# Kernel optimization log

Hardware: AMD Instinct MI355X
Metric: run time of the kernel (lower is better)

The kernel has to match this reference:

```python
import jax, jax.numpy as jnp
import numpy as np

B, L, H, E = 16, 4096, 8, 64
K = 64  # topk modes
SCALE = 1.0 / (512 * 512)  # 1/(in_channels*out_channels)


def setup_inputs() -> dict:
    key = jax.random.key(0)
    k1, k2, k3 = jax.random.split(key, 3)
    q = jax.random.normal(k1, (B, L, H, E), dtype=jnp.float32)
    k = jnp.zeros((B, L, H, E), jnp.float32)  # unused by module
    v = jnp.zeros((B, L, H, E), jnp.float32)  # unused by module
    mask = jnp.zeros((1,), jnp.int32)         # unused by module
    w_real = jax.random.uniform(k2, (K, H, E, E), dtype=jnp.float32) * SCALE
    w_imag = jax.random.uniform(k3, (K, H, E, E), dtype=jnp.float32) * SCALE
    return {"q": q, "k": k, "v": v, "w_real": w_real, "w_imag": w_imag, "mask": mask}


def reference(q, k, v, w_real, w_imag, mask):
    # x_ft: (B, F, H, Ein) complex64, F = L//2 + 1
    x_ft = jnp.fft.rfft(q.astype(jnp.float32), axis=1)
    F = x_ft.shape[1]
    kk = w_real.shape[0]
    # energy score per bin: sum |.|^2 over Ein, mean over batch, mean over heads
    e = (x_ft.real ** 2 + x_ft.imag ** 2).sum(-1)      # (B, F, H)
    score = e.mean(0).mean(-1)                          # (F,)
    score = score.at[0].set(-jnp.inf)                   # topk_exclude_dc=True
    _, idx = jax.lax.top_k(score, kk)                   # sorted desc by energy
    # gather selected modes: (B, K, H, Ein)
    x_sel = x_ft[:, idx]
    w = jax.lax.complex(w_real, w_imag)                 # (K, H, Ein, Eout)
    out_sel = jnp.einsum('bkhe,khef->bkhf', x_sel, w)   # per-head complex matmul
    # packed scatter: selected modes written into the first K bins of zero spectrum
    out_ft = jnp.zeros((x_ft.shape[0], F, x_ft.shape[2], w.shape[-1]), jnp.complex64)
    out_ft = out_ft.at[:, :kk].set(out_sel)
    # inverse FFT back to time domain, norm='backward' (default)
    return jnp.fft.irfft(out_ft, n=q.shape[1], axis=1)
```

## Files before the change

### kernel.cpp

```cpp
#include <hip/hip_runtime.h>


#define NTHREADS 256

__device__ inline void lds_barrier() {
    asm volatile("s_waitcnt lgkmcnt(0)" ::: "memory");
    __builtin_amdgcn_s_barrier();
}

#define ZI(i) ((i) ^ ((((i) >> 4) & 7) << 1))

__device__ inline float2 f2add(float2 a, float2 b) { return make_float2(a.x + b.x, a.y + b.y); }
__device__ inline float2 f2sub(float2 a, float2 b) { return make_float2(a.x - b.x, a.y - b.y); }
__device__ inline float2 cmulf(float2 a, float2 b) {
    return make_float2(__builtin_fmaf(a.x, b.x, -(a.y * b.y)),
                       __builtin_fmaf(a.x, b.y,  a.y * b.x));
}

__device__ inline void radix8(float2& u0, float2& u1, float2& u2, float2& u3,
                              float2& u4, float2& u5, float2& u6, float2& u7,
                              float2 wA, float2 wB, float2 wC) {
    float2 t1 = cmulf(wA, u1), t3 = cmulf(wA, u3), t5 = cmulf(wA, u5), t7 = cmulf(wA, u7);
    float2 a0 = f2add(u0, t1), a1 = f2sub(u0, t1);
    float2 a2 = f2add(u2, t3), a3 = f2sub(u2, t3);
    float2 a4 = f2add(u4, t5), a5 = f2sub(u4, t5);
    float2 a6 = f2add(u6, t7), a7 = f2sub(u6, t7);
    float2 s2 = cmulf(wB, a2), s3 = cmulf(wB, a3);
    float2 s6 = cmulf(wB, a6), s7 = cmulf(wB, a7);
    float2 b0 = f2add(a0, s2), b2 = f2sub(a0, s2);
    float2 b1 = make_float2(a1.x + s3.y, a1.y - s3.x);
    float2 b3 = make_float2(a1.x - s3.y, a1.y + s3.x);
    float2 b4 = f2add(a4, s6), b6 = f2sub(a4, s6);
    float2 b5 = make_float2(a5.x + s7.y, a5.y - s7.x);
    float2 b7 = make_float2(a5.x - s7.y, a5.y + s7.x);
    const float2 C8 = make_float2(0.70710678118654752f, -0.70710678118654752f);
    float2 wC1 = cmulf(wC, C8);
    float2 r4 = cmulf(wC, b4);
    float2 r5 = cmulf(wC1, b5);
    float2 r6t = cmulf(wC, b6);  float2 r6 = make_float2(r6t.y, -r6t.x);
    float2 r7t = cmulf(wC1, b7); float2 r7 = make_float2(r7t.y, -r7t.x);
    u0 = f2add(b0, r4); u4 = f2sub(b0, r4);
    u1 = f2add(b1, r5); u5 = f2sub(b1, r5);
    u2 = f2add(b2, r6); u6 = f2sub(b2, r6);
    u3 = f2add(b3, r7); u7 = f2sub(b3, r7);
}

__global__ void k_tables(float2* __restrict__ trig) {
    int k = blockIdx.x * blockDim.x + threadIdx.x;
    if (k < 4096) {
        double th = (6.283185307179586476925286766559 * (double)k) / 4096.0;
        trig[k] = make_float2((float)cos(th), (float)sin(th));
    }
}

__global__ __launch_bounds__(256) void k_xpose(const float* __restrict__ q,
                                               float2* __restrict__ T) {
    __shared__ float tile[128][65];

    const int tid = threadIdx.x;
    const int bi  = blockIdx.x;
    const int b   = bi >> 8;
    const int h   = (bi >> 5) & 7;
    const int c5  = bi & 31;

    const float* qb = q + ((size_t)b * 4096 * 512) + (size_t)h * 64;
#pragma unroll
    for (int i = 0; i < 8; ++i) {
        const int f = tid + 256 * i;
        const int t = f >> 4, e4 = f & 15;
        const float4 v = *(const float4*)(qb + (size_t)(c5 + 32 * t) * 512 + e4 * 4);
        tile[t][e4 * 4 + 0] = v.x;
        tile[t][e4 * 4 + 1] = v.y;
        tile[t][e4 * 4 + 2] = v.z;
        tile[t][e4 * 4 + 3] = v.w;
    }
    lds_barrier();

    const int wave = tid >> 6, lane = tid & 63;
    const int rl  = __brev(lane) >> 26;
    const int r5c = __brev(c5) >> 27;
    for (int cc = wave; cc < 32; cc += 4) {
        const int eo = cc >> 2, p = cc & 3;
        const int col0 = eo * 8 + 2 * p;
        float2* dst = T + ((size_t)((b * 8 + h) * 8 + eo)) * 16384 + (size_t)p * 4096
                        + (size_t)r5c * 128;
        float4 o;
        o.x = tile[rl][col0];      o.y = tile[rl][col0 + 1];
        o.z = tile[rl + 64][col0]; o.w = tile[rl + 64][col0 + 1];
        *(float4*)(dst + 2 * lane) = o;
    }
}

__global__ __launch_bounds__(256) void k_fft(const float2* __restrict__ trig,
                                             float2* __restrict__ Xout,
                                             unsigned long long* __restrict__ score) {
    __shared__ float2 z[4096];
    __shared__ float2 ctw[216];

    const int tid = threadIdx.x;
    const int bi  = blockIdx.x;

    if (tid < 72) {
        int off, j, sA;
        if (tid < 8) { off = 0;  j = tid;     sA = 8; }
        else         { off = 24; j = tid - 8; sA = 5; }
        float2 a = trig[j << sA], b = trig[j << (sA - 1)], c = trig[j << (sA - 2)];
        ctw[off + 3 * j + 0] = make_float2(a.x, -a.y);
        ctw[off + 3 * j + 1] = make_float2(b.x, -b.y);
        ctw[off + 3 * j + 2] = make_float2(c.x, -c.y);
    }

    float eaccr[8];
#pragma unroll
    for (int k = 0; k < 8; ++k) eaccr[k] = 0.f;

    const float2 ONE = make_float2(1.0f, 0.0f);
    const float2* base = Xout + (size_t)bi * 16384;

    float4 pre[2][4];
#pragma unroll
    for (int it = 0; it < 2; ++it) {
        const int t = tid + 256 * it;
#pragma unroll
        for (int g = 0; g < 4; ++g) pre[it][g] = *(const float4*)(base + 8 * t + 2 * g);
    }
    lds_barrier();

    for (int p = 0; p < 4; ++p) {
        float4 cur[2][4];
#pragma unroll
        for (int it = 0; it < 2; ++it)
#pragma unroll
            for (int g = 0; g < 4; ++g) cur[it][g] = pre[it][g];

        if (p < 3) {
            const float2* pn = base + (size_t)(p + 1) * 4096;
#pragma unroll
            for (int it = 0; it < 2; ++it) {
                const int t = tid + 256 * it;
#pragma unroll
                for (int g = 0; g < 4; ++g) pre[it][g] = *(const float4*)(pn + 8 * t + 2 * g);
            }
        }

#pragma unroll
        for (int it = 0; it < 2; ++it) {
            const int t = tid + 256 * it;
            float2 u0 = make_float2(cur[it][0].x, cur[it][0].y);
            float2 u1 = make_float2(cur[it][0].z, cur[it][0].w);
            float2 u2 = make_float2(cur[it][1].x, cur[it][1].y);
            float2 u3 = make_float2(cur[it][1].z, cur[it][1].w);
            float2 u4 = make_float2(cur[it][2].x, cur[it][2].y);
            float2 u5 = make_float2(cur[it][2].z, cur[it][2].w);
            float2 u6 = make_float2(cur[it][3].x, cur[it][3].y);
            float2 u7 = make_float2(cur[it][3].z, cur[it][3].w);
            radix8(u0, u1, u2, u3, u4, u5, u6, u7, ONE, ONE, ONE);
            const int i0 = 8 * t;
            z[ZI(i0 + 0)] = u0; z[ZI(i0 + 1)] = u1; z[ZI(i0 + 2)] = u2; z[ZI(i0 + 3)] = u3;
            z[ZI(i0 + 4)] = u4; z[ZI(i0 + 5)] = u5; z[ZI(i0 + 6)] = u6; z[ZI(i0 + 7)] = u7;
        }
        lds_barrier();

#pragma unroll
        for (int p8 = 1; p8 <= 3; ++p8) {
            const int st  = 1 + 3 * p8;
            const int h   = 1 << (st - 1);
            for (int t = tid; t < 512; t += NTHREADS) {
                const int j = t & (h - 1);
                const int g = t >> (st - 1);
                const int i0 = (g << (st + 2)) + j;
                int a0 = ZI(i0),         a1 = ZI(i0 + h),     a2 = ZI(i0 + 2 * h), a3 = ZI(i0 + 3 * h);
                int a4 = ZI(i0 + 4 * h), a5 = ZI(i0 + 5 * h), a6 = ZI(i0 + 6 * h), a7 = ZI(i0 + 7 * h);
                float2 u0 = z[a0], u1 = z[a1], u2 = z[a2], u3 = z[a3];
                float2 u4 = z[a4], u5 = z[a5], u6 = z[a6], u7 = z[a7];
                float2 wA, wB, wC;
                if (p8 < 3) {
                    const int off = (p8 == 1) ? 0 : 24;
                    wA = ctw[off + 3 * j + 0];
                    wB = ctw[off + 3 * j + 1];
                    wC = ctw[off + 3 * j + 2];
                } else {
                    float2 a = trig[j << 2], b = trig[j << 1], c = trig[j];
                    wA = make_float2(a.x, -a.y);
                    wB = make_float2(b.x, -b.y);
                    wC = make_float2(c.x, -c.y);
                }
                radix8(u0, u1, u2, u3, u4, u5, u6, u7, wA, wB, wC);
                z[a0] = u0; z[a1] = u1; z[a2] = u2; z[a3] = u3;
                z[a4] = u4; z[a5] = u5; z[a6] = u6; z[a7] = u7;
            }
            lds_barrier();
        }

        {
            const size_t s0 = (size_t)bi * 16384 + (size_t)p * 4096;
#pragma unroll
            for (int k = 0; k < 8; ++k) {
                const int t = tid + 256 * k;
                const int m = t + 1;
                float2 Za = z[ZI(m)];
                float2 Zb = z[ZI(4096 - m)];
                float Xr0 = 0.5f * (Za.x + Zb.x);
                float Xi0 = 0.5f * (Za.y - Zb.y);
                float Xr1 = 0.5f * (Za.y + Zb.y);
                float Xi1 = 0.5f * (Zb.x - Za.x);
                Xout[s0 + t]        = make_float2(Xr0, Xi0);
                Xout[s0 + 2048 + t] = make_float2(Xr1, Xi1);
                eaccr[k] += Xr0 * Xr0 + Xi0 * Xi0 + Xr1 * Xr1 + Xi1 * Xi1;
            }
        }
        lds_barrier();
    }

#pragma unroll
    for (int k = 0; k < 8; ++k) {
        unsigned long long v = (unsigned long long)llrintf(eaccr[k] * 1048576.0f);
        atomicAdd(&score[tid + 256 * k], v);
    }
}

__global__ __launch_bounds__(256) void k_topk(const unsigned long long* __restrict__ score,
                                              int* __restrict__ idx) {
    __shared__ unsigned long long s[2048];
    const int tid = threadIdx.x;
    for (int t = tid; t < 2048; t += 256) s[t] = score[t];
    __syncthreads();

    const int t = blockIdx.x * 256 + tid;
    const unsigned long long my = s[t];
    int rank = 0;
#pragma unroll 8
    for (int u = 0; u < 2048; ++u) {
        unsigned long long o = s[u];
        rank += (int)((o > my) || (o == my && u < t));
    }
    if (rank < 64) idx[rank] = t + 1;
}

__global__ __launch_bounds__(256) void k_proj(const float2* __restrict__ X,
                                              const float* __restrict__ wr,
                                              const float* __restrict__ wi,
                                              const int* __restrict__ idx,
                                              float2* __restrict__ Y) {
    __shared__ float2 xs[16 * 64];
    __shared__ float  wrs[64 * 64];
    __shared__ float  wis[64 * 64];

    const int tid = threadIdx.x;
    const int j = blockIdx.x >> 3;
    const int h = blockIdx.x & 7;
    const int m = idx[j];

    for (int t = tid; t < 1024; t += NTHREADS) {
        int b = t >> 6, e = t & 63;
        xs[t] = X[((size_t)((b * 8 + h) * 64 + e)) * 2048 + (size_t)(m - 1)];
    }
    const float* wrb = wr + ((size_t)(j * 8 + h)) * 4096;
    const float* wib = wi + ((size_t)(j * 8 + h)) * 4096;
    for (int t = tid; t < 4096; t += NTHREADS) { wrs[t] = wrb[t]; wis[t] = wib[t]; }
    lds_barrier();

    const int b  = tid >> 4;
    const int fg = tid & 15;
    for (int fo = 0; fo < 4; ++fo) {
        int f = fg * 4 + fo;
        float yr = 0.f, yi = 0.f;
        for (int e = 0; e < 64; ++e) {
            float2 x = xs[b * 64 + e];
            float a = wrs[e * 64 + f], c = wis[e * 64 + f];
            yr = __builtin_fmaf(x.x, a, yr); yr = __builtin_fmaf(-x.y, c, yr);
            yi = __builtin_fmaf(x.x, c, yi); yi = __builtin_fmaf( x.y, a, yi);
        }
        Y[((size_t)b * 64 + j) * 512 + (size_t)(h * 64 + f)] = make_float2(yr, yi);
    }
}

__global__ __launch_bounds__(256, 4) void k_synth(const float2* __restrict__ Y,
                                                  const float2* __restrict__ trig,
                                                  float* __restrict__ out) {
    __shared__ __align__(16) float2 ys[64][32];

    const int tid = threadIdx.x;
    const int bi  = blockIdx.x;
    const int b   = bi >> 8;
    const int hft = (bi >> 4) & 15;
    const int lt  = bi & 15;

    const float invN = 1.0f / 4096.0f;
    const float2* yb = Y + (size_t)b * 64 * 512 + (size_t)hft * 32;
    for (int t = tid; t < 64 * 32; t += NTHREADS) {
        int j = t >> 5, cc = t & 31;
        float2 y = yb[(size_t)j * 512 + cc];
        if (j == 0) ys[0][cc] = make_float2(y.x * invN, 0.0f);
        else        ys[j][cc] = make_float2(y.x * (2.0f * invN), y.y * (2.0f * invN));
    }
    lds_barrier();

    const int r = tid >> 3;
    const int c = tid & 7;
    const int l0 = lt * 64 + r * 2;

    float2 rot[2], w[2];
#pragma unroll
    for (int v = 0; v < 2; ++v) {
        w[v] = trig[(l0 + v) & 4095];
        rot[v] = make_float2(1.0f, 0.0f);
    }

    float F0[2][4], F1[2][4], F2[2][4], F3[2][4], H1[2][4], H3[2][4];
#pragma unroll
    for (int v = 0; v < 2; ++v)
#pragma unroll
        for (int u = 0; u < 4; ++u) {
            F0[v][u] = F1[v][u] = F2[v][u] = F3[v][u] = 0.0f;
            H1[v][u] = H3[v][u] = 0.0f;
        }

#define LOAD_YV(JROW)                                                        \
    float2 yv[4];                                                            \
    {                                                                        \
        const float4 ta = *(const float4*)&ys[(JROW)][c * 2];                \
        const float4 tb = *(const float4*)&ys[(JROW)][c * 2 + 16];           \
        yv[0] = make_float2(ta.x, ta.y); yv[1] = make_float2(ta.z, ta.w);    \
        yv[2] = make_float2(tb.x, tb.y); yv[3] = make_float2(tb.z, tb.w);    \
    }

    for (int j = 0; j < 64; j += 4) {
        {
            LOAD_YV(j)
#pragma unroll
            for (int v = 0; v < 2; ++v) {
                const float cx = rot[v].x, sx = rot[v].y;
#pragma unroll
                for (int u = 0; u < 4; ++u) {
                    float a = F0[v][u];
                    a = __builtin_fmaf(cx, yv[u].x, a);
                    a = __builtin_fmaf(-sx, yv[u].y, a);
                    F0[v][u] = a;
                }
                float nx = __builtin_fmaf(rot[v].x, w[v].x, -(rot[v].y * w[v].y));
                float ny = __builtin_fmaf(rot[v].x, w[v].y,  (rot[v].y * w[v].x));
                rot[v] = make_float2(nx, ny);
            }
        }
        {
            LOAD_YV(j + 1)
#pragma unroll
            for (int v = 0; v < 2; ++v) {
                const float cx = rot[v].x, sx = rot[v].y;
#pragma unroll
                for (int u = 0; u < 4; ++u) {
                    float a = F1[v][u], g = H1[v][u];
                    a = __builtin_fmaf(cx, yv[u].x, a);
                    a = __builtin_fmaf(-sx, yv[u].y, a);
                    g = __builtin_fmaf(sx, yv[u].x, g);
                    g = __builtin_fmaf(cx, yv[u].y, g);
                    F1[v][u] = a; H1[v][u] = g;
                }
                float nx = __builtin_fmaf(rot[v].x, w[v].x, -(rot[v].y * w[v].y));
                float ny = __builtin_fmaf(rot[v].x, w[v].y,  (rot[v].y * w[v].x));
                rot[v] = make_float2(nx, ny);
            }
        }
        {
            LOAD_YV(j + 2)
#pragma unroll
            for (int v = 0; v < 2; ++v) {
                const float cx = rot[v].x, sx = rot[v].y;
#pragma unroll
                for (int u = 0; u < 4; ++u) {
                    float a = F2[v][u];
                    a = __builtin_fmaf(cx, yv[u].x, a);
                    a = __builtin_fmaf(-sx, yv[u].y, a);
                    F2[v][u] = a;
                }
                float nx = __builtin_fmaf(rot[v].x, w[v].x, -(rot[v].y * w[v].y));
                float ny = __builtin_fmaf(rot[v].x, w[v].y,  (rot[v].y * w[v].x));
                rot[v] = make_float2(nx, ny);
            }
        }
        {
            LOAD_YV(j + 3)
#pragma unroll
            for (int v = 0; v < 2; ++v) {
                const float cx = rot[v].x, sx = rot[v].y;
#pragma unroll
                for (int u = 0; u < 4; ++u) {
                    float a = F3[v][u], g = H3[v][u];
                    a = __builtin_fmaf(cx, yv[u].x, a);
                    a = __builtin_fmaf(-sx, yv[u].y, a);
                    g = __builtin_fmaf(sx, yv[u].x, g);
                    g = __builtin_fmaf(cx, yv[u].y, g);
                    F3[v][u] = a; H3[v][u] = g;
                }
                float nx = __builtin_fmaf(rot[v].x, w[v].x, -(rot[v].y * w[v].y));
                float ny = __builtin_fmaf(rot[v].x, w[v].y,  (rot[v].y * w[v].x));
                rot[v] = make_float2(nx, ny);
            }
        }
    }
#undef LOAD_YV

#pragma unroll
    for (int v = 0; v < 2; ++v) {
        float* o0 = out + ((size_t)(b * 4096 + l0 + v)) * 512 + (size_t)hft * 32;
        float* o1 = o0 + (size_t)1024 * 512;
        float* o2 = o0 + (size_t)2048 * 512;
        float* o3 = o0 + (size_t)3072 * 512;
#pragma unroll
        for (int k = 0; k < 2; ++k) {
            float2 s0, s1, s2, s3;
#pragma unroll
            for (int d = 0; d < 2; ++d) {
                const int u = 2 * k + d;
                const float p = F0[v][u] + F2[v][u];
                const float m = F0[v][u] - F2[v][u];
                const float q = F1[v][u] + F3[v][u];
                const float hh = H3[v][u] - H1[v][u];
                ((float*)&s0)[d] = p + q;
                ((float*)&s2)[d] = p - q;
                ((float*)&s1)[d] = m + hh;
                ((float*)&s3)[d] = m - hh;
            }
            *(float2*)(o0 + k * 16 + c * 2) = s0;
            *(float2*)(o1 + k * 16 + c * 2) = s1;
            *(float2*)(o2 + k * 16 + c * 2) = s2;
            *(float2*)(o3 + k * 16 + c * 2) = s3;
        }
    }
}

extern "C" void kernel_launch(void* const* d_in, const int* in_sizes, int n_in,
                              void* d_out, int out_size, void* d_ws, size_t ws_size,
                              hipStream_t stream) {
    const float* q  = (const float*)d_in[0];
    const float* wr = (const float*)d_in[3];
    const float* wi = (const float*)d_in[4];

    char* ws = (char*)d_ws;
    float2*             trig  = (float2*)(ws + 0);
    unsigned long long* score = (unsigned long long*)(ws + 32768);
    int*                idx   = (int*)(ws + 49152);
    float2*             Y     = (float2*)(ws + 65536);

    float2* Xs = (float2*)d_out;

    hipMemsetAsync(score, 0, 2048 * sizeof(unsigned long long), stream);
    k_tables<<<16, 256, 0, stream>>>(trig);
    k_xpose<<<4096, 256, 0, stream>>>(q, Xs);
    k_fft<<<1024, 256, 0, stream>>>(trig, Xs, score);
    k_topk<<<8, 256, 0, stream>>>(score, idx);
    k_proj<<<512, 256, 0, stream>>>(Xs, wr, wi, idx, Y);
    k_synth<<<4096, 256, 0, stream>>>(Y, trig, (float*)d_out);
}
```

Baseline: 249.6 us.

## Replace radix-8 FFT passes with three radix-16 passes in forward FFT

Restructures the 4096-point LDS FFT from four radix-8 passes (two loop iterations per thread) into three radix-16 passes with one 16-point butterfly per thread. This removes one LDS read/write pass and one barrier per transform, and lets the first pass write to LDS with float4 stores. The cost is more registers per thread (16 complex values plus prefetch buffers), which may lower occupancy. Twiddle tables are rebuilt for the new stage layout.

```diff
diff --git a/kernel.cpp b/kernel.cpp
--- a/kernel.cpp
+++ b/kernel.cpp
@@ -17,32 +17,71 @@
                        __builtin_fmaf(a.x, b.y,  a.y * b.x));
 }
 
-__device__ inline void radix8(float2& u0, float2& u1, float2& u2, float2& u3,
-                              float2& u4, float2& u5, float2& u6, float2& u7,
-                              float2 wA, float2 wB, float2 wC) {
-    float2 t1 = cmulf(wA, u1), t3 = cmulf(wA, u3), t5 = cmulf(wA, u5), t7 = cmulf(wA, u7);
-    float2 a0 = f2add(u0, t1), a1 = f2sub(u0, t1);
-    float2 a2 = f2add(u2, t3), a3 = f2sub(u2, t3);
-    float2 a4 = f2add(u4, t5), a5 = f2sub(u4, t5);
-    float2 a6 = f2add(u6, t7), a7 = f2sub(u6, t7);
-    float2 s2 = cmulf(wB, a2), s3 = cmulf(wB, a3);
-    float2 s6 = cmulf(wB, a6), s7 = cmulf(wB, a7);
-    float2 b0 = f2add(a0, s2), b2 = f2sub(a0, s2);
-    float2 b1 = make_float2(a1.x + s3.y, a1.y - s3.x);
-    float2 b3 = make_float2(a1.x - s3.y, a1.y + s3.x);
-    float2 b4 = f2add(a4, s6), b6 = f2sub(a4, s6);
-    float2 b5 = make_float2(a5.x + s7.y, a5.y - s7.x);
-    float2 b7 = make_float2(a5.x - s7.y, a5.y + s7.x);
-    const float2 C8 = make_float2(0.70710678118654752f, -0.70710678118654752f);
-    float2 wC1 = cmulf(wC, C8);
-    float2 r4 = cmulf(wC, b4);
-    float2 r5 = cmulf(wC1, b5);
-    float2 r6t = cmulf(wC, b6);  float2 r6 = make_float2(r6t.y, -r6t.x);
-    float2 r7t = cmulf(wC1, b7); float2 r7 = make_float2(r7t.y, -r7t.x);
-    u0 = f2add(b0, r4); u4 = f2sub(b0, r4);
-    u1 = f2add(b1, r5); u5 = f2sub(b1, r5);
-    u2 = f2add(b2, r6); u6 = f2sub(b2, r6);
-    u3 = f2add(b3, r7); u7 = f2sub(b3, r7);
+__device__ inline void radix16(float2 x[16], float2 tA, float2 tB, float2 tC, float2 tD) {
+#pragma unroll
+    for (int q = 0; q < 8; ++q) {
+        float2 v = cmulf(tA, x[2 * q + 1]);
+        float2 u = x[2 * q];
+        x[2 * q]     = f2add(u, v);
+        x[2 * q + 1] = f2sub(u, v);
+    }
+    {
+        float2 tB1 = make_float2(tB.y, -tB.x);
+#pragma unroll
+        for (int q = 0; q < 4; ++q) {
+            {
+                float2 v = cmulf(tB, x[4 * q + 2]);
+                float2 u = x[4 * q];
+                x[4 * q]     = f2add(u, v);
+                x[4 * q + 2] = f2sub(u, v);
+            }
+            {
+                float2 v = cmulf(tB1, x[4 * q + 3]);
+                float2 u = x[4 * q + 1];
+                x[4 * q + 1] = f2add(u, v);
+                x[4 * q + 3] = f2sub(u, v);
+            }
+        }
+    }
+    {
+        const float C = 0.70710678118654752f;
+        float2 w0 = tC;
+        float2 w1 = cmulf(tC, make_float2(C, -C));
+        float2 w2 = make_float2(tC.y, -tC.x);
+        float2 w3 = cmulf(tC, make_float2(-C, -C));
+#pragma unroll
+        for (int q = 0; q < 2; ++q) {
+            float2 ws[4] = {w0, w1, w2, w3};
+#pragma unroll
+            for (int r = 0; r < 4; ++r) {
+                float2 v = cmulf(ws[r], x[8 * q + r + 4]);
+                float2 u = x[8 * q + r];
+                x[8 * q + r]     = f2add(u, v);
+                x[8 * q + r + 4] = f2sub(u, v);
+            }
+        }
+    }
+    {
+        const float C  = 0.70710678118654752f;
+        const float C1 = 0.92387953251128676f;
+        const float S1 = 0.38268343236508977f;
+        float2 wD[8];
+        wD[0] = tD;
+        wD[1] = cmulf(tD, make_float2(C1, -S1));
+        wD[2] = cmulf(tD, make_float2(C, -C));
+        wD[3] = cmulf(tD, make_float2(S1, -C1));
+        wD[4] = make_float2(tD.y, -tD.x);
+        wD[5] = cmulf(tD, make_float2(-S1, -C1));
+        wD[6] = cmulf(tD, make_float2(-C, -C));
+        wD[7] = cmulf(tD, make_float2(-C1, -S1));
+#pragma unroll
+        for (int r = 0; r < 8; ++r) {
+            float2 v = cmulf(wD[r], x[r + 8]);
+            float2 u = x[r];
+            x[r]     = f2add(u, v);
+            x[r + 8] = f2sub(u, v);
+        }
+    }
 }
 
 __global__ void k_tables(float2* __restrict__ trig) {
@@ -95,19 +134,15 @@
                                              float2* __restrict__ Xout,
                                              unsigned long long* __restrict__ score) {
     __shared__ float2 z[4096];
-    __shared__ float2 ctw[216];
+    __shared__ float2 ctw4[80];
 
     const int tid = threadIdx.x;
     const int bi  = blockIdx.x;
 
-    if (tid < 72) {
-        int off, j, sA;
-        if (tid < 8) { off = 0;  j = tid;     sA = 8; }
-        else         { off = 24; j = tid - 8; sA = 5; }
-        float2 a = trig[j << sA], b = trig[j << (sA - 1)], c = trig[j << (sA - 2)];
-        ctw[off + 3 * j + 0] = make_float2(a.x, -a.y);
-        ctw[off + 3 * j + 1] = make_float2(b.x, -b.y);
-        ctw[off + 3 * j + 2] = make_float2(c.x, -c.y);
+    if (tid < 64) {
+        const int j = tid >> 2, qq = tid & 3;
+        float2 a = trig[j << (7 - qq)];
+        ctw4[5 * j + qq] = make_float2(a.x, -a.y);
     }
 
     float eaccr[8];
@@ -117,80 +152,71 @@
     const float2 ONE = make_float2(1.0f, 0.0f);
     const float2* base = Xout + (size_t)bi * 16384;
 
-    float4 pre[2][4];
-#pragma unroll
-    for (int it = 0; it < 2; ++it) {
-        const int t = tid + 256 * it;
-#pragma unroll
-        for (int g = 0; g < 4; ++g) pre[it][g] = *(const float4*)(base + 8 * t + 2 * g);
-    }
+    float4 pre[8];
+#pragma unroll
+    for (int g = 0; g < 8; ++g) pre[g] = *(const float4*)(base + 16 * tid + 2 * g);
     lds_barrier();
 
     for (int p = 0; p < 4; ++p) {
-        float4 cur[2][4];
-#pragma unroll
-        for (int it = 0; it < 2; ++it)
-#pragma unroll
-            for (int g = 0; g < 4; ++g) cur[it][g] = pre[it][g];
-
+        float2 x[16];
+#pragma unroll
+        for (int g = 0; g < 8; ++g) {
+            x[2 * g]     = make_float2(pre[g].x, pre[g].y);
+            x[2 * g + 1] = make_float2(pre[g].z, pre[g].w);
+        }
         if (p < 3) {
             const float2* pn = base + (size_t)(p + 1) * 4096;
 #pragma unroll
-            for (int it = 0; it < 2; ++it) {
-                const int t = tid + 256 * it;
-#pragma unroll
-                for (int g = 0; g < 4; ++g) pre[it][g] = *(const float4*)(pn + 8 * t + 2 * g);
-            }
-        }
-
-#pragma unroll
-        for (int it = 0; it < 2; ++it) {
-            const int t = tid + 256 * it;
-            float2 u0 = make_float2(cur[it][0].x, cur[it][0].y);
-            float2 u1 = make_float2(cur[it][0].z, cur[it][0].w);
-            float2 u2 = make_float2(cur[it][1].x, cur[it][1].y);
-            float2 u3 = make_float2(cur[it][1].z, cur[it][1].w);
-            float2 u4 = make_float2(cur[it][2].x, cur[it][2].y);
-            float2 u5 = make_float2(cur[it][2].z, cur[it][2].w);
-            float2 u6 = make_float2(cur[it][3].x, cur[it][3].y);
-            float2 u7 = make_float2(cur[it][3].z, cur[it][3].w);
-            radix8(u0, u1, u2, u3, u4, u5, u6, u7, ONE, ONE, ONE);
-            const int i0 = 8 * t;
-            z[ZI(i0 + 0)] = u0; z[ZI(i0 + 1)] = u1; z[ZI(i0 + 2)] = u2; z[ZI(i0 + 3)] = u3;
-            z[ZI(i0 + 4)] = u4; z[ZI(i0 + 5)] = u5; z[ZI(i0 + 6)] = u6; z[ZI(i0 + 7)] = u7;
+            for (int g = 0; g < 8; ++g) pre[g] = *(const float4*)(pn + 16 * tid + 2 * g);
+        }
+
+        radix16(x, ONE, ONE, ONE, ONE);
+        {
+            const int i0 = 16 * tid;
+#pragma unroll
+            for (int s = 0; s < 8; ++s) {
+                *(float4*)&z[ZI(i0 + 2 * s)] = make_float4(x[2 * s].x, x[2 * s].y,
+                                                           x[2 * s + 1].x, x[2 * s + 1].y);
+            }
         }
         lds_barrier();
 
-#pragma unroll
-        for (int p8 = 1; p8 <= 3; ++p8) {
-            const int st  = 1 + 3 * p8;
-            const int h   = 1 << (st - 1);
-            for (int t = tid; t < 512; t += NTHREADS) {
-                const int j = t & (h - 1);
-                const int g = t >> (st - 1);
-                const int i0 = (g << (st + 2)) + j;
-                int a0 = ZI(i0),         a1 = ZI(i0 + h),     a2 = ZI(i0 + 2 * h), a3 = ZI(i0 + 3 * h);
-                int a4 = ZI(i0 + 4 * h), a5 = ZI(i0 + 5 * h), a6 = ZI(i0 + 6 * h), a7 = ZI(i0 + 7 * h);
-                float2 u0 = z[a0], u1 = z[a1], u2 = z[a2], u3 = z[a3];
-                float2 u4 = z[a4], u5 = z[a5], u6 = z[a6], u7 = z[a7];
-                float2 wA, wB, wC;
-                if (p8 < 3) {
-                    const int off = (p8 == 1) ? 0 : 24;
-                    wA = ctw[off + 3 * j + 0];
-                    wB = ctw[off + 3 * j + 1];
-                    wC = ctw[off + 3 * j + 2];
-                } else {
-                    float2 a = trig[j << 2], b = trig[j << 1], c = trig[j];
-                    wA = make_float2(a.x, -a.y);
-                    wB = make_float2(b.x, -b.y);
-                    wC = make_float2(c.x, -c.y);
-                }
-                radix8(u0, u1, u2, u3, u4, u5, u6, u7, wA, wB, wC);
-                z[a0] = u0; z[a1] = u1; z[a2] = u2; z[a3] = u3;
-                z[a4] = u4; z[a5] = u5; z[a6] = u6; z[a7] = u7;
-            }
-            lds_barrier();
-        }
+        {
+            const int j = tid & 15;
+            const int g = tid >> 4;
+            const int i0 = (g << 8) + j;
+            int ad[16];
+#pragma unroll
+            for (int k = 0; k < 16; ++k) ad[k] = ZI(i0 + 16 * k);
+#pragma unroll
+            for (int k = 0; k < 16; ++k) x[k] = z[ad[k]];
+            const float2 tA = ctw4[5 * j + 0];
+            const float2 tB = ctw4[5 * j + 1];
+            const float2 tC = ctw4[5 * j + 2];
+            const float2 tD = ctw4[5 * j + 3];
+            radix16(x, tA, tB, tC, tD);
+#pragma unroll
+            for (int k = 0; k < 16; ++k) z[ad[k]] = x[k];
+        }
+        lds_barrier();
+
+        {
+            const int j = tid;
+            int ad[16];
+#pragma unroll
+            for (int k = 0; k < 16; ++k) ad[k] = ZI(j + 256 * k);
+#pragma unroll
+            for (int k = 0; k < 16; ++k) x[k] = z[ad[k]];
+            float2 a = trig[j << 3], b2 = trig[j << 2], c = trig[j << 1], d = trig[j];
+            const float2 tA = make_float2(a.x, -a.y);
+            const float2 tB = make_float2(b2.x, -b2.y);
+            const float2 tC = make_float2(c.x, -c.y);
+            const float2 tD = make_float2(d.x, -d.y);
+            radix16(x, tA, tB, tC, tD);
+#pragma unroll
+            for (int k = 0; k < 16; ++k) z[ad[k]] = x[k];
+        }
+        lds_barrier();
 
         {
             const size_t s0 = (size_t)bi * 16384 + (size_t)p * 4096;
```

New measurement: 247.0 us. No clear change (-1.0%).
